# Optimization experiments

Measured on AMD Instinct MI355X. Metric: run time of the kernel, lower is better.

The kernel has to match this reference:

```python
import jax, jax.numpy as jnp
import numpy as np

N_SLOTS = 64
DECAY = 0.999
B, S, H, M = 4, 4096, 2048, 128


def _l2norm(t, eps=1e-12):
    return t / jnp.maximum(jnp.linalg.norm(t, axis=-1, keepdims=True), eps)


def setup_inputs() -> dict:
    key = jax.random.key(0)
    ks = jax.random.split(key, 6)
    return {
        "x": jax.random.normal(ks[0], (B, S, H), dtype=jnp.float32),
        "W_query": jax.random.normal(ks[1], (M, H), dtype=jnp.float32) * 0.02,
        "W_key": jax.random.normal(ks[2], (M, H), dtype=jnp.float32) * 0.02,
        "W_value": jax.random.normal(ks[3], (M, H), dtype=jnp.float32) * 0.02,
        "W_out": jax.random.normal(ks[4], (H, M), dtype=jnp.float32) * 0.02,
        "W_gate_w": jax.random.normal(ks[5], (1, H), dtype=jnp.float32) * 0.02,
        "W_gate_b": jnp.full((1,), -2.0, dtype=jnp.float32),
        "log_beta": jnp.full((1,), np.log(8.0), dtype=jnp.float32),
        "chunk_size": 64,
    }


def reference(x, W_query, W_key, W_value, W_out, W_gate_w, W_gate_b, log_beta, chunk_size):
    b, s, h = x.shape
    m = W_query.shape[0]
    dt = x.dtype

    q = x @ W_query.T                      # (b, s, m)
    k = _l2norm(x @ W_key.T)               # (b, s, m)
    v = _l2norm(x @ W_value.T)             # (b, s, m)
    gate = jax.nn.sigmoid(x @ W_gate_w.T + W_gate_b)  # (b, s, 1)
    beta = jnp.exp(log_beta).reshape(())

    nc = s // chunk_size
    decay_c = jnp.asarray(DECAY, dt) ** chunk_size

    def chunkify(t):
        # (b, s, d) -> (nc, b, chunk, d)
        return jnp.moveaxis(t.reshape(b, nc, chunk_size, -1), 1, 0)

    qc, kc, vc = chunkify(q), chunkify(k), chunkify(v)
    wc = chunkify(gate)[..., 0]            # (nc, b, chunk)

    K0 = jnp.zeros((N_SLOTS, m), dt)
    V0 = jnp.zeros((N_SLOTS, m), dt)
    s0 = jnp.zeros((N_SLOTS,), dt)
    ptr0 = jnp.asarray(0, jnp.int32)

    def step(carry, inp):
        K_mem, V_mem, mem_strength, ptr = carry
        qch, kch, vch, wch = inp           # (b,c,m) x3, (b,c)
        # --- read: softmax retrieval over active slots ---
        slot_mask = (mem_strength > 1e-8).astype(dt)           # (n_slots,)
        scores = jnp.einsum("bcm,nm->bcn", qch, K_mem) * beta
        scores = scores + (1.0 - slot_mask) * -1e9
        attn = jax.nn.softmax(scores, axis=-1)
        r = jnp.einsum("bcn,nm->bcm", attn, V_mem)
        r = jnp.where(mem_strength.sum() < 1e-8, jnp.zeros_like(r), r)
        # --- write: gated aggregation into one slot ---
        w_sum = jnp.maximum(wch.sum(), 1e-8)
        k_agg = _l2norm((kch * wch[..., None]).sum((0, 1)) / w_sum)
        v_agg = _l2norm((vch * wch[..., None]).sum((0, 1)) / w_sum)
        write_str = wch.mean()
        mem_strength = mem_strength * decay_c
        slot = ptr % N_SLOTS
        K_mem = K_mem.at[slot].set(k_agg)
        V_mem = V_mem.at[slot].set(v_agg)
        mem_strength = mem_strength.at[slot].set(write_str)
        return (K_mem, V_mem, mem_strength, ptr + 1), (r, write_str)

    _, (rs, wss) = jax.lax.scan(step, (K0, V0, s0, ptr0), (qc, kc, vc, wc))

    retrieved = jnp.moveaxis(rs, 0, 1).reshape(b, s, m)
    out = retrieved @ W_out.T              # (b, s, h)
    # clamp output norm to 10
    onorm = jnp.maximum(jnp.linalg.norm(out, axis=-1, keepdims=True), 1e-6)
    out = out * jnp.minimum(10.0 / onorm, 1.0)
    mean_ws = jnp.mean(wss)
    return out, mean_ws
```

## Files before the change

### kernel.cpp

```cpp
#include <hip/hip_runtime.h>
#include <math.h>
#include <stdint.h>

#define NTOK 16384
#define SEQ  4096
#define HD   2048
#define MD   128
#define NCH  64
#define CHK  64

typedef __attribute__((ext_vector_type(8))) _Float16 half8;
typedef __attribute__((ext_vector_type(4))) float floatx4;

__device__ __forceinline__ void gload_lds16(const void* g, void* l) {
    __builtin_amdgcn_global_load_lds(
        (const __attribute__((address_space(1))) unsigned int*)(uintptr_t)g,
        (__attribute__((address_space(3))) unsigned int*)(uintptr_t)l,
        16, 0, 0);
}

__global__ __launch_bounds__(256) void convert_w_kernel(
    const float* __restrict__ Wq, const float* __restrict__ Wk,
    const float* __restrict__ Wv, const float* __restrict__ Wo,
    _Float16* __restrict__ Wcath, _Float16* __restrict__ Woh)
{
    int i = blockIdx.x * 256 + threadIdx.x;
    if (i < 384 * HD) {
        int r = i >> 11;
        float val;
        if (r < 128)      val = Wq[i];
        else if (r < 256) val = Wk[i - 128 * HD];
        else              val = Wv[i - 256 * HD];
        Wcath[i] = (_Float16)val;
    } else {
        int j = i - 384 * HD;
        Woh[j] = (_Float16)Wo[j];
    }
}

__global__ __launch_bounds__(128) void gmat_kernel(
    const float* __restrict__ Wo, float* __restrict__ G)
{
    __shared__ float col[HD];
    int a = blockIdx.x;
    int b = threadIdx.x;
    for (int j = b; j < HD; j += 128) col[j] = Wo[(size_t)j * MD + a];
    __syncthreads();
    float s = 0.f;
    for (int j = 0; j < HD; ++j) s = fmaf(col[j], Wo[(size_t)j * MD + b], s);
    G[a * MD + b] = s;
}

__global__ __launch_bounds__(256, 3) void gemm_proj_mfma(
    const float* __restrict__ x, const _Float16* __restrict__ Wcath,
    const float* __restrict__ Wgw, const float* __restrict__ gb,
    float* __restrict__ q, float* __restrict__ k, float* __restrict__ v,
    float* __restrict__ wg)
{
    __shared__ _Float16 As[2][64 * 64];
    __shared__ _Float16 Bs[2][128 * 64];
    floatx4 acc[2][4];
    #pragma unroll
    for (int i = 0; i < 2; ++i)
        #pragma unroll
        for (int j = 0; j < 4; ++j) acc[i][j] = (floatx4){0.f, 0.f, 0.f, 0.f};

    const int tid  = threadIdx.x;
    const int wave = tid >> 6, lane = tid & 63;
    const int wm = wave & 1, wn = wave >> 1;
    const int row0 = blockIdx.x * 64;
    const int col0 = blockIdx.y * 128;
    const bool do_gate = (blockIdx.y == 0);

    const int ar0 = tid >> 3;
    const int ac0 = (tid & 7) ^ (ar0 & 7);
    const float* xA0 = x + (size_t)(row0 + ar0) * HD + ac0 * 8;
    const float* xA1 = x + (size_t)(row0 + ar0 + 32) * HD + ac0 * 8;
    const float* wgp = Wgw + ac0 * 8;

    float gacc0 = 0.f, gacc1 = 0.f;
    float4 a00, a01, a10, a11, g0, g1;

#define STAGE_B(buf_, k0_) do {                                               \
        _Pragma("unroll")                                                     \
        for (int rnd = 0; rnd < 4; ++rnd) {                                   \
            int sg = rnd * 4 + wave;                                          \
            int br = sg * 8 + (lane >> 3);                                    \
            int bc = (lane & 7) ^ (br & 7);                                   \
            gload_lds16(Wcath + (size_t)(col0 + br) * HD + (k0_) + bc * 8,    \
                        (char*)Bs[buf_] + sg * 1024);                         \
        } } while (0)

#define LOAD_A(k0_) do {                                                      \
        a00 = *(const float4*)(xA0 + (k0_));                                  \
        a01 = *(const float4*)(xA0 + (k0_) + 4);                              \
        a10 = *(const float4*)(xA1 + (k0_));                                  \
        a11 = *(const float4*)(xA1 + (k0_) + 4);                              \
        if (do_gate) {                                                        \
            g0 = *(const float4*)(wgp + (k0_));                               \
            g1 = *(const float4*)(wgp + (k0_) + 4);                           \
        } } while (0)

#define FINISH_A(buf_) do {                                                   \
        if (do_gate) {                                                        \
            gacc0 += a00.x*g0.x + a00.y*g0.y + a00.z*g0.z + a00.w*g0.w        \
                   + a01.x*g1.x + a01.y*g1.y + a01.z*g1.z + a01.w*g1.w;       \
            gacc1 += a10.x*g0.x + a10.y*g0.y + a10.z*g0.z + a10.w*g0.w        \
                   + a11.x*g1.x + a11.y*g1.y + a11.z*g1.z + a11.w*g1.w;       \
        }                                                                     \
        half8 h0, h1;                                                         \
        h0[0] = (_Float16)a00.x; h0[1] = (_Float16)a00.y;                     \
        h0[2] = (_Float16)a00.z; h0[3] = (_Float16)a00.w;                     \
        h0[4] = (_Float16)a01.x; h0[5] = (_Float16)a01.y;                     \
        h0[6] = (_Float16)a01.z; h0[7] = (_Float16)a01.w;                     \
        h1[0] = (_Float16)a10.x; h1[1] = (_Float16)a10.y;                     \
        h1[2] = (_Float16)a10.z; h1[3] = (_Float16)a10.w;                     \
        h1[4] = (_Float16)a11.x; h1[5] = (_Float16)a11.y;                     \
        h1[6] = (_Float16)a11.z; h1[7] = (_Float16)a11.w;                     \
        *(half8*)((char*)As[buf_] + tid * 16)        = h0;                    \
        *(half8*)((char*)As[buf_] + 4096 + tid * 16) = h1;                    \
    } while (0)

#define COMPUTE(buf_) do {                                                    \
        half8 af[2][2], bf[4][2];                                             \
        _Pragma("unroll")                                                     \
        for (int i = 0; i < 2; ++i) {                                         \
            int r  = wm * 32 + i * 16 + (lane & 15);                          \
            int rb = r * 128 + (lane >> 4) * 16;                              \
            int sw = (r & 7) << 4;                                            \
            af[i][0] = *(const half8*)((const char*)As[buf_] + ( rb       ^ sw)); \
            af[i][1] = *(const half8*)((const char*)As[buf_] + ((rb + 64) ^ sw)); \
        }                                                                     \
        _Pragma("unroll")                                                     \
        for (int j = 0; j < 4; ++j) {                                         \
            int r  = wn * 64 + j * 16 + (lane & 15);                          \
            int rb = r * 128 + (lane >> 4) * 16;                              \
            int sw = (r & 7) << 4;                                            \
            bf[j][0] = *(const half8*)((const char*)Bs[buf_] + ( rb       ^ sw)); \
            bf[j][1] = *(const half8*)((const char*)Bs[buf_] + ((rb + 64) ^ sw)); \
        }                                                                     \
        _Pragma("unroll")                                                     \
        for (int ks = 0; ks < 2; ++ks)                                        \
            _Pragma("unroll")                                                 \
            for (int i = 0; i < 2; ++i)                                       \
                _Pragma("unroll")                                             \
                for (int j = 0; j < 4; ++j)                                   \
                    acc[i][j] = __builtin_amdgcn_mfma_f32_16x16x32_f16(       \
                        af[i][ks], bf[j][ks], acc[i][j], 0, 0, 0);            \
    } while (0)

    STAGE_B(0, 0);
    LOAD_A(0);
    FINISH_A(0);
    __syncthreads();

    int cur = 0;
    for (int t = 0; t < HD / 64; ++t) {
        if (t < HD / 64 - 1) {
            STAGE_B(cur ^ 1, (t + 1) * 64);
            LOAD_A((t + 1) * 64);
        }
        COMPUTE(cur);
        if (t < HD / 64 - 1) FINISH_A(cur ^ 1);
        __syncthreads();
        cur ^= 1;
    }

    if (do_gate) {
        gacc0 += __shfl_xor(gacc0, 1);
        gacc0 += __shfl_xor(gacc0, 2);
        gacc0 += __shfl_xor(gacc0, 4);
        gacc1 += __shfl_xor(gacc1, 1);
        gacc1 += __shfl_xor(gacc1, 2);
        gacc1 += __shfl_xor(gacc1, 4);
        if ((tid & 7) == 0) {
            wg[row0 + ar0]      = 1.f / (1.f + expf(-(gacc0 + gb[0])));
            wg[row0 + ar0 + 32] = 1.f / (1.f + expf(-(gacc1 + gb[0])));
        }
    }

    float* dst = (blockIdx.y == 0) ? q : ((blockIdx.y == 1) ? k : v);
    #pragma unroll
    for (int i = 0; i < 2; ++i) {
        int m = row0 + wm * 32 + i * 16 + (lane >> 4) * 4;
        #pragma unroll
        for (int j = 0; j < 4; ++j) {
            int c = wn * 64 + j * 16 + (lane & 15);
            #pragma unroll
            for (int r = 0; r < 4; ++r)
                dst[(size_t)(m + r) * MD + c] = acc[i][j][r];
        }
    }
#undef STAGE_B
#undef LOAD_A
#undef FINISH_A
#undef COMPUTE
}

__global__ __launch_bounds__(256) void normsig_kernel(
    float* __restrict__ k, float* __restrict__ v)
{
    int wave = threadIdx.x >> 6, lane = threadIdx.x & 63;
    int row = blockIdx.x * 4 + wave;
    size_t base = (size_t)row * MD + lane * 2;
    float2 k2 = *reinterpret_cast<float2*>(&k[base]);
    float2 v2 = *reinterpret_cast<float2*>(&v[base]);
    float ks = k2.x * k2.x + k2.y * k2.y;
    float vs = v2.x * v2.x + v2.y * v2.y;
    #pragma unroll
    for (int off = 32; off > 0; off >>= 1) {
        ks += __shfl_xor(ks, off);
        vs += __shfl_xor(vs, off);
    }
    float ki = 1.f / fmaxf(sqrtf(ks), 1e-12f);
    float vi = 1.f / fmaxf(sqrtf(vs), 1e-12f);
    k2.x *= ki; k2.y *= ki; v2.x *= vi; v2.y *= vi;
    *reinterpret_cast<float2*>(&k[base]) = k2;
    *reinterpret_cast<float2*>(&v[base]) = v2;
}

__global__ __launch_bounds__(256) void agg_part_kernel(
    const float* __restrict__ kn, const float* __restrict__ vn,
    const float* __restrict__ w,
    float* __restrict__ kpart, float* __restrict__ vpart,
    float* __restrict__ wpart)
{
    int t = blockIdx.x >> 2, b = blockIdx.x & 3;
    int tid = threadIdx.x;
    int d = tid & 127, h = tid >> 7;
    int base_row = b * SEQ + t * CHK;

    float ka = 0.f, va = 0.f;
    for (int c = h * 32; c < h * 32 + 32; ++c) {
        int row = base_row + c;
        float wv = w[row];
        ka = fmaf(wv, kn[(size_t)row * MD + d], ka);
        va = fmaf(wv, vn[(size_t)row * MD + d], va);
    }
    __shared__ float sk[128], sv[128];
    if (h == 1) { sk[d] = ka; sv[d] = va; }
    __syncthreads();
    if (h == 0) {
        kpart[(size_t)blockIdx.x * 128 + d] = ka + sk[d];
        vpart[(size_t)blockIdx.x * 128 + d] = va + sv[d];
    }
    if (tid < 64) {
        float wv = w[base_row + tid];
        #pragma unroll
        for (int off = 32; off > 0; off >>= 1) wv += __shfl_xor(wv, off);
        if (tid == 0) wpart[blockIdx.x] = wv;
    }
}

__global__ __launch_bounds__(128) void agg_combine_kernel(
    const float* __restrict__ kpart, const float* __restrict__ vpart,
    const float* __restrict__ wpart,
    float* __restrict__ kaT, float* __restrict__ vagg, float* __restrict__ wstr)
{
    int t = blockIdx.x;
    int d = threadIdx.x;
    int wave = d >> 6, lane = d & 63;
    float ku = 0.f, vu = 0.f;
    #pragma unroll
    for (int b = 0; b < 4; ++b) {
        ku += kpart[(size_t)(t * 4 + b) * 128 + d];
        vu += vpart[(size_t)(t * 4 + b) * 128 + d];
    }
    float wsum = wpart[t * 4] + wpart[t * 4 + 1] + wpart[t * 4 + 2] + wpart[t * 4 + 3];
    float winv = 1.f / fmaxf(wsum, 1e-8f);
    ku *= winv; vu *= winv;

    __shared__ float red[4];
    float ks = ku * ku, vs = vu * vu;
    #pragma unroll
    for (int off = 32; off > 0; off >>= 1) {
        ks += __shfl_xor(ks, off);
        vs += __shfl_xor(vs, off);
    }
    if (lane == 0) { red[wave] = ks; red[2 + wave] = vs; }
    __syncthreads();
    float kinv = 1.f / fmaxf(sqrtf(red[0] + red[1]), 1e-12f);
    float vinv = 1.f / fmaxf(sqrtf(red[2] + red[3]), 1e-12f);
    kaT[d * NCH + t] = ku * kinv;
    vagg[t * MD + d] = vu * vinv;
    if (d == 0) wstr[t] = wsum * (1.f / 256.f);
}

__global__ __launch_bounds__(64) void meanws_kernel(
    const float* __restrict__ wstr, float* __restrict__ outp)
{
    int lane = threadIdx.x;
    float v = wstr[lane];
    #pragma unroll
    for (int off = 32; off > 0; off >>= 1) v += __shfl_xor(v, off);
    if (lane == 0) outp[0] = v * (1.f / 64.f);
}

__global__ __launch_bounds__(512, 1) void attn_kernel(
    const float* __restrict__ q, const float* __restrict__ kaT,
    const float* __restrict__ vagg, const float* __restrict__ G,
    const float* __restrict__ logbeta, _Float16* __restrict__ rsh16)
{
    __shared__ float kaT_s[MD * NCH];
    __shared__ float vagg_s[NCH * MD];
    __shared__ float G_s[MD * MD];
    __shared__ float qs[8][MD];
    __shared__ float attn_sh[8][64];
    __shared__ float rsh_sh[8][MD];

    const int tid  = threadIdx.x;
    const int wave = tid >> 6, lane = tid & 63;
    const int row0 = blockIdx.x * 64;
    const int t = (row0 & (SEQ - 1)) >> 6;
    const float beta = expf(logbeta[0]);

    {
        const float4* s0 = (const float4*)kaT;
        const float4* s1 = (const float4*)vagg;
        const float4* s2 = (const float4*)G;
        float4* d0 = (float4*)kaT_s;
        float4* d1 = (float4*)vagg_s;
        float4* d2 = (float4*)G_s;
        #pragma unroll
        for (int i = 0; i < 4; ++i) {
            d0[tid + i * 512] = s0[tid + i * 512];
            d1[tid + i * 512] = s1[tid + i * 512];
        }
        #pragma unroll
        for (int i = 0; i < 8; ++i)
            d2[tid + i * 512] = s2[tid + i * 512];
    }
    __syncthreads();

    for (int rr = 0; rr < 8; ++rr) {
        const int row = row0 + wave * 8 + rr;
        float q0 = q[(size_t)row * MD + lane];
        float q1 = q[(size_t)row * MD + 64 + lane];
        qs[wave][lane]      = q0;
        qs[wave][lane + 64] = q1;

        float sc = -INFINITY;
        if (lane < t) {
            sc = 0.f;
            for (int d = 0; d < 128; ++d)
                sc = fmaf(qs[wave][d], kaT_s[d * NCH + lane], sc);
            sc *= beta;
        }
        float mx = sc;
        #pragma unroll
        for (int off = 32; off > 0; off >>= 1) mx = fmaxf(mx, __shfl_xor(mx, off));
        float e = (lane < t) ? expf(sc - mx) : 0.f;
        float ssum = e;
        #pragma unroll
        for (int off = 32; off > 0; off >>= 1) ssum += __shfl_xor(ssum, off);
        float attn = (t > 0) ? (e / ssum) : 0.f;
        attn_sh[wave][lane] = attn;

        float r0 = 0.f, r1 = 0.f;
        for (int n = 0; n < t; ++n) {
            float a = attn_sh[wave][n];
            r0 = fmaf(a, vagg_s[n * MD + lane], r0);
            r1 = fmaf(a, vagg_s[n * MD + 64 + lane], r1);
        }
        rsh_sh[wave][lane]      = r0;
        rsh_sh[wave][lane + 64] = r1;

        float t0 = 0.f, t1 = 0.f;
        for (int b = 0; b < 128; ++b) {
            float rb = rsh_sh[wave][b];
            t0 = fmaf(G_s[b * MD + lane], rb, t0);
            t1 = fmaf(G_s[b * MD + 64 + lane], rb, t1);
        }
        float quad = r0 * t0 + r1 * t1;
        #pragma unroll
        for (int off = 32; off > 0; off >>= 1) quad += __shfl_xor(quad, off);
        float nrm = fmaxf(sqrtf(fmaxf(quad, 0.f)), 1e-6f);
        float scl = fminf(10.f / nrm, 1.f);
        rsh16[(size_t)row * MD + lane]      = (_Float16)(r0 * scl);
        rsh16[(size_t)row * MD + 64 + lane] = (_Float16)(r1 * scl);
    }
}

__global__ __launch_bounds__(256) void gemm_out_mfma(
    const _Float16* __restrict__ rsh16, const _Float16* __restrict__ Woh,
    float* __restrict__ C)
{
    __shared__ _Float16 As[128 * 128];
    __shared__ _Float16 Bs[128 * 128];
    floatx4 acc[4][4];
    #pragma unroll
    for (int i = 0; i < 4; ++i)
        #pragma unroll
        for (int j = 0; j < 4; ++j) acc[i][j] = (floatx4){0.f, 0.f, 0.f, 0.f};

    const int tid  = threadIdx.x;
    const int wave = tid >> 6, lane = tid & 63;
    const int wm = wave & 1, wn = wave >> 1;
    const int row0 = blockIdx.x * 128;
    const int col0 = blockIdx.y * 128;

    const int sr = lane >> 4;
    const int sp = lane & 15;
    #pragma unroll
    for (int rnd = 0; rnd < 8; ++rnd) {
        int seg = wave * 8 + rnd;
        int r = seg * 4 + sr;
        int c = sp ^ (r & 15);
        gload_lds16(rsh16 + (size_t)(row0 + r) * MD + c * 8,
                    (char*)As + seg * 1024);
        gload_lds16(Woh + (size_t)(col0 + r) * MD + c * 8,
                    (char*)Bs + seg * 1024);
    }
    __syncthreads();

    #pragma unroll
    for (int kf = 0; kf < 4; ++kf) {
        half8 af[4], bf[4];
        #pragma unroll
        for (int i = 0; i < 4; ++i) {
            int r = wm * 64 + i * 16 + (lane & 15);
            int g = kf * 4 + (lane >> 4);
            af[i] = *(const half8*)((const char*)As + r * 256 + ((g ^ (r & 15)) * 16));
        }
        #pragma unroll
        for (int j = 0; j < 4; ++j) {
            int r = wn * 64 + j * 16 + (lane & 15);
            int g = kf * 4 + (lane >> 4);
            bf[j] = *(const half8*)((const char*)Bs + r * 256 + ((g ^ (r & 15)) * 16));
        }
        #pragma unroll
        for (int i = 0; i < 4; ++i)
            #pragma unroll
            for (int j = 0; j < 4; ++j)
                acc[i][j] = __builtin_amdgcn_mfma_f32_16x16x32_f16(
                    af[i], bf[j], acc[i][j], 0, 0, 0);
    }

    #pragma unroll
    for (int i = 0; i < 4; ++i) {
        int m = row0 + wm * 64 + i * 16 + (lane >> 4) * 4;
        #pragma unroll
        for (int j = 0; j < 4; ++j) {
            int c = col0 + wn * 64 + j * 16 + (lane & 15);
            #pragma unroll
            for (int r = 0; r < 4; ++r)
                C[(size_t)(m + r) * HD + c] = acc[i][j][r];
        }
    }
}

extern "C" void kernel_launch(void* const* d_in, const int* in_sizes, int n_in,
                              void* d_out, int out_size, void* d_ws, size_t ws_size,
                              hipStream_t stream)
{
    const float* x   = (const float*)d_in[0];
    const float* Wq  = (const float*)d_in[1];
    const float* Wk  = (const float*)d_in[2];
    const float* Wv  = (const float*)d_in[3];
    const float* Wo  = (const float*)d_in[4];
    const float* Wgw = (const float*)d_in[5];
    const float* Wgb = (const float*)d_in[6];
    const float* lb  = (const float*)d_in[7];
    float* out = (float*)d_out;

    float* q    = (float*)d_ws;
    float* kn   = q + (size_t)NTOK * MD;
    float* vn   = kn + (size_t)NTOK * MD;
    float* wg   = vn + (size_t)NTOK * MD;
    float* kaT  = wg + NTOK;
    float* vagg = kaT + MD * NCH;
    float* wstr = vagg + NCH * MD;
    float* G    = wstr + 64;
    float* kpart = G + MD * MD;
    float* vpart = kpart + 256 * 128;
    float* wpart = vpart + 256 * 128;
    _Float16* Wcath = (_Float16*)(wpart + 256);
    _Float16* Woh   = Wcath + 384 * HD;
    _Float16* rsh16 = Woh + HD * MD;

    convert_w_kernel<<<dim3(4096), dim3(256), 0, stream>>>(Wq, Wk, Wv, Wo, Wcath, Woh);
    gmat_kernel<<<dim3(128), dim3(128), 0, stream>>>(Wo, G);
    gemm_proj_mfma<<<dim3(NTOK / 64, 3), dim3(256), 0, stream>>>(
        x, Wcath, Wgw, Wgb, q, kn, vn, wg);
    normsig_kernel<<<dim3(NTOK / 4), dim3(256), 0, stream>>>(kn, vn);
    agg_part_kernel<<<dim3(256), dim3(256), 0, stream>>>(kn, vn, wg, kpart, vpart, wpart);
    agg_combine_kernel<<<dim3(NCH), dim3(128), 0, stream>>>(kpart, vpart, wpart, kaT, vagg, wstr);
    meanws_kernel<<<dim3(1), dim3(64), 0, stream>>>(wstr, out + (size_t)NTOK * HD);
    attn_kernel<<<dim3(NTOK / 64), dim3(512), 0, stream>>>(q, kaT, vagg, G, lb, rsh16);
    gemm_out_mfma<<<dim3(NTOK / 128, HD / 128), dim3(256), 0, stream>>>(rsh16, Woh, out);
}
```

Before: 390.3 us.

## Compute all three Q/K/V projections per block to read x only once

```diff
diff --git a/kernel.cpp b/kernel.cpp
--- a/kernel.cpp
+++ b/kernel.cpp
@@ -51,26 +51,26 @@
     G[a * MD + b] = s;
 }
 
-__global__ __launch_bounds__(256, 3) void gemm_proj_mfma(
+__global__ __launch_bounds__(256, 1) void gemm_proj_mfma(
     const float* __restrict__ x, const _Float16* __restrict__ Wcath,
     const float* __restrict__ Wgw, const float* __restrict__ gb,
     float* __restrict__ q, float* __restrict__ k, float* __restrict__ v,
     float* __restrict__ wg)
 {
     __shared__ _Float16 As[2][64 * 64];
-    __shared__ _Float16 Bs[2][128 * 64];
-    floatx4 acc[2][4];
-    #pragma unroll
-    for (int i = 0; i < 2; ++i)
-        #pragma unroll
-        for (int j = 0; j < 4; ++j) acc[i][j] = (floatx4){0.f, 0.f, 0.f, 0.f};
+    __shared__ _Float16 Bs[2][3][128 * 64];
+    floatx4 acc[3][2][4];
+    #pragma unroll
+    for (int p = 0; p < 3; ++p)
+        #pragma unroll
+        for (int i = 0; i < 2; ++i)
+            #pragma unroll
+            for (int j = 0; j < 4; ++j) acc[p][i][j] = (floatx4){0.f, 0.f, 0.f, 0.f};
 
     const int tid  = threadIdx.x;
     const int wave = tid >> 6, lane = tid & 63;
     const int wm = wave & 1, wn = wave >> 1;
     const int row0 = blockIdx.x * 64;
-    const int col0 = blockIdx.y * 128;
-    const bool do_gate = (blockIdx.y == 0);
 
     const int ar0 = tid >> 3;
     const int ac0 = (tid & 7) ^ (ar0 & 7);
@@ -83,12 +83,15 @@
 
 #define STAGE_B(buf_, k0_) do {                                               \
         _Pragma("unroll")                                                     \
-        for (int rnd = 0; rnd < 4; ++rnd) {                                   \
-            int sg = rnd * 4 + wave;                                          \
-            int br = sg * 8 + (lane >> 3);                                    \
-            int bc = (lane & 7) ^ (br & 7);                                   \
-            gload_lds16(Wcath + (size_t)(col0 + br) * HD + (k0_) + bc * 8,    \
-                        (char*)Bs[buf_] + sg * 1024);                         \
+        for (int p = 0; p < 3; ++p) {                                         \
+            _Pragma("unroll")                                                 \
+            for (int rnd = 0; rnd < 4; ++rnd) {                               \
+                int sg = rnd * 4 + wave;                                      \
+                int br = sg * 8 + (lane >> 3);                                \
+                int bc = (lane & 7) ^ (br & 7);                               \
+                gload_lds16(Wcath + (size_t)(p * 128 + br) * HD + (k0_) + bc * 8, \
+                            (char*)Bs[buf_][p] + sg * 1024);                  \
+            }                                                                 \
         } } while (0)
 
 #define LOAD_A(k0_) do {                                                      \
@@ -96,18 +99,15 @@
         a01 = *(const float4*)(xA0 + (k0_) + 4);                              \
         a10 = *(const float4*)(xA1 + (k0_));                                  \
         a11 = *(const float4*)(xA1 + (k0_) + 4);                              \
-        if (do_gate) {                                                        \
-            g0 = *(const float4*)(wgp + (k0_));                               \
-            g1 = *(const float4*)(wgp + (k0_) + 4);                           \
-        } } while (0)
+        g0 = *(const float4*)(wgp + (k0_));                                   \
+        g1 = *(const float4*)(wgp + (k0_) + 4);                               \
+    } while (0)
 
 #define FINISH_A(buf_) do {                                                   \
-        if (do_gate) {                                                        \
-            gacc0 += a00.x*g0.x + a00.y*g0.y + a00.z*g0.z + a00.w*g0.w        \
-                   + a01.x*g1.x + a01.y*g1.y + a01.z*g1.z + a01.w*g1.w;       \
-            gacc1 += a10.x*g0.x + a10.y*g0.y + a10.z*g0.z + a10.w*g0.w        \
-                   + a11.x*g1.x + a11.y*g1.y + a11.z*g1.z + a11.w*g1.w;       \
-        }                                                                     \
+        gacc0 += a00.x*g0.x + a00.y*g0.y + a00.z*g0.z + a00.w*g0.w            \
+               + a01.x*g1.x + a01.y*g1.y + a01.z*g1.z + a01.w*g1.w;           \
+        gacc1 += a10.x*g0.x + a10.y*g0.y + a10.z*g0.z + a10.w*g0.w            \
+               + a11.x*g1.x + a11.y*g1.y + a11.z*g1.z + a11.w*g1.w;           \
         half8 h0, h1;                                                         \
         h0[0] = (_Float16)a00.x; h0[1] = (_Float16)a00.y;                     \
         h0[2] = (_Float16)a00.z; h0[3] = (_Float16)a00.w;                     \
@@ -122,7 +122,7 @@
     } while (0)
 
 #define COMPUTE(buf_) do {                                                    \
-        half8 af[2][2], bf[4][2];                                             \
+        half8 af[2][2];                                                       \
         _Pragma("unroll")                                                     \
         for (int i = 0; i < 2; ++i) {                                         \
             int r  = wm * 32 + i * 16 + (lane & 15);                          \
@@ -132,21 +132,25 @@
             af[i][1] = *(const half8*)((const char*)As[buf_] + ((rb + 64) ^ sw)); \
         }                                                                     \
         _Pragma("unroll")                                                     \
-        for (int j = 0; j < 4; ++j) {                                         \
-            int r  = wn * 64 + j * 16 + (lane & 15);                          \
-            int rb = r * 128 + (lane >> 4) * 16;                              \
-            int sw = (r & 7) << 4;                                            \
-            bf[j][0] = *(const half8*)((const char*)Bs[buf_] + ( rb       ^ sw)); \
-            bf[j][1] = *(const half8*)((const char*)Bs[buf_] + ((rb + 64) ^ sw)); \
+        for (int p = 0; p < 3; ++p) {                                         \
+            half8 bf[4][2];                                                   \
+            _Pragma("unroll")                                                 \
+            for (int j = 0; j < 4; ++j) {                                     \
+                int r  = wn * 64 + j * 16 + (lane & 15);                      \
+                int rb = r * 128 + (lane >> 4) * 16;                          \
+                int sw = (r & 7) << 4;                                        \
+                bf[j][0] = *(const half8*)((const char*)Bs[buf_][p] + ( rb       ^ sw)); \
+                bf[j][1] = *(const half8*)((const char*)Bs[buf_][p] + ((rb + 64) ^ sw)); \
+            }                                                                 \
+            _Pragma("unroll")                                                 \
+            for (int ks = 0; ks < 2; ++ks)                                    \
+                _Pragma("unroll")                                             \
+                for (int i = 0; i < 2; ++i)                                   \
+                    _Pragma("unroll")                                         \
+                    for (int j = 0; j < 4; ++j)                               \
+                        acc[p][i][j] = __builtin_amdgcn_mfma_f32_16x16x32_f16(\
+                            af[i][ks], bf[j][ks], acc[p][i][j], 0, 0, 0);     \
         }                                                                     \
-        _Pragma("unroll")                                                     \
-        for (int ks = 0; ks < 2; ++ks)                                        \
-            _Pragma("unroll")                                                 \
-            for (int i = 0; i < 2; ++i)                                       \
-                _Pragma("unroll")                                             \
-                for (int j = 0; j < 4; ++j)                                   \
-                    acc[i][j] = __builtin_amdgcn_mfma_f32_16x16x32_f16(       \
-                        af[i][ks], bf[j][ks], acc[i][j], 0, 0, 0);            \
     } while (0)
 
     STAGE_B(0, 0);
@@ -166,29 +170,30 @@
         cur ^= 1;
     }
 
-    if (do_gate) {
-        gacc0 += __shfl_xor(gacc0, 1);
-        gacc0 += __shfl_xor(gacc0, 2);
-        gacc0 += __shfl_xor(gacc0, 4);
-        gacc1 += __shfl_xor(gacc1, 1);
-        gacc1 += __shfl_xor(gacc1, 2);
-        gacc1 += __shfl_xor(gacc1, 4);
-        if ((tid & 7) == 0) {
-            wg[row0 + ar0]      = 1.f / (1.f + expf(-(gacc0 + gb[0])));
-            wg[row0 + ar0 + 32] = 1.f / (1.f + expf(-(gacc1 + gb[0])));
-        }
-    }
-
-    float* dst = (blockIdx.y == 0) ? q : ((blockIdx.y == 1) ? k : v);
-    #pragma unroll
-    for (int i = 0; i < 2; ++i) {
-        int m = row0 + wm * 32 + i * 16 + (lane >> 4) * 4;
-        #pragma unroll
-        for (int j = 0; j < 4; ++j) {
-            int c = wn * 64 + j * 16 + (lane & 15);
+    gacc0 += __shfl_xor(gacc0, 1);
+    gacc0 += __shfl_xor(gacc0, 2);
+    gacc0 += __shfl_xor(gacc0, 4);
+    gacc1 += __shfl_xor(gacc1, 1);
+    gacc1 += __shfl_xor(gacc1, 2);
+    gacc1 += __shfl_xor(gacc1, 4);
+    if ((tid & 7) == 0) {
+        wg[row0 + ar0]      = 1.f / (1.f + expf(-(gacc0 + gb[0])));
+        wg[row0 + ar0 + 32] = 1.f / (1.f + expf(-(gacc1 + gb[0])));
+    }
+
+    #pragma unroll
+    for (int p = 0; p < 3; ++p) {
+        float* dst = (p == 0) ? q : ((p == 1) ? k : v);
+        #pragma unroll
+        for (int i = 0; i < 2; ++i) {
+            int m = row0 + wm * 32 + i * 16 + (lane >> 4) * 4;
             #pragma unroll
-            for (int r = 0; r < 4; ++r)
-                dst[(size_t)(m + r) * MD + c] = acc[i][j][r];
+            for (int j = 0; j < 4; ++j) {
+                int c = wn * 64 + j * 16 + (lane & 15);
+                #pragma unroll
+                for (int r = 0; r < 4; ++r)
+                    dst[(size_t)(m + r) * MD + c] = acc[p][i][j][r];
+            }
         }
     }
 #undef STAGE_B
@@ -480,7 +485,7 @@
 
     convert_w_kernel<<<dim3(4096), dim3(256), 0, stream>>>(Wq, Wk, Wv, Wo, Wcath, Woh);
     gmat_kernel<<<dim3(128), dim3(128), 0, stream>>>(Wo, G);
-    gemm_proj_mfma<<<dim3(NTOK / 64, 3), dim3(256), 0, stream>>>(
+    gemm_proj_mfma<<<dim3(NTOK / 64), dim3(256), 0, stream>>>(
         x, Wcath, Wgw, Wgb, q, kn, vn, wg);
     normsig_kernel<<<dim3(NTOK / 4), dim3(256), 0, stream>>>(kn, vn);
     agg_part_kernel<<<dim3(256), dim3(256), 0, stream>>>(kn, vn, wg, kpart, vpart, wpart);
```

After: 393.5 us. No clear change (+0.8%).
